# Kernel tuning notes

Hardware: AMD Instinct MI355X
Metric: run time of the kernel (lower is better)

## Reference

```python
import jax, jax.numpy as jnp
import numpy as np

N_NODES = 100000
N_EDGES = 1600000
IN_DIM = 128
HID = 64
N_CLASSES = 40
NEG_SLOPE = 0.2


def setup_inputs() -> dict:
    key = jax.random.key(0)
    ks = jax.random.split(key, 12)
    s_in = 1.0 / np.sqrt(IN_DIM)
    s_h = 1.0 / np.sqrt(HID)
    return {
        "x": jax.random.normal(ks[0], (N_NODES, IN_DIM), dtype=jnp.float32),
        "edge_index": jax.random.randint(ks[1], (2, N_EDGES), 0, N_NODES, dtype=jnp.int64),
        "W0": jax.random.normal(ks[2], (IN_DIM, HID), dtype=jnp.float32) * s_in,
        "a_s0": jax.random.normal(ks[3], (HID,), dtype=jnp.float32) * s_h,
        "a_d0": jax.random.normal(ks[4], (HID,), dtype=jnp.float32) * s_h,
        "b0": jnp.zeros((HID,), dtype=jnp.float32),
        "W1": jax.random.normal(ks[5], (HID, HID), dtype=jnp.float32) * s_h,
        "a_s1": jax.random.normal(ks[6], (HID,), dtype=jnp.float32) * s_h,
        "a_d1": jax.random.normal(ks[7], (HID,), dtype=jnp.float32) * s_h,
        "b1": jnp.zeros((HID,), dtype=jnp.float32),
        "Wl": jax.random.normal(ks[8], (HID, N_CLASSES), dtype=jnp.float32) * s_h,
        "bl": jnp.zeros((N_CLASSES,), dtype=jnp.float32),
    }


def gat_conv(x, src, dst, W, a_s, a_d, b, n_nodes):
    # single-head GATConv (PyG default heads=1), self-loops already in src/dst
    h = x @ W                                  # [N, d]
    e = jax.nn.leaky_relu((h @ a_s)[src] + (h @ a_d)[dst], NEG_SLOPE)  # [E]
    # segment softmax over incoming edges of each dst node
    m = jax.ops.segment_max(e, dst, num_segments=n_nodes)
    p = jnp.exp(e - m[dst])
    denom = jax.ops.segment_sum(p, dst, num_segments=n_nodes)
    alpha = p / (denom[dst] + 1e-16)           # [E]
    out = jax.ops.segment_sum(alpha[:, None] * h[src], dst, num_segments=n_nodes)
    return out + b


def reference(x, edge_index, W0, a_s0, a_d0, b0, W1, a_s1, a_d1, b1, Wl, bl):
    n = x.shape[0]
    loop = jnp.arange(n, dtype=edge_index.dtype)
    src = jnp.concatenate([edge_index[0], loop])
    dst = jnp.concatenate([edge_index[1], loop])
    h = gat_conv(x, src, dst, W0, a_s0, a_d0, b0, n)
    h = jax.nn.elu(h)
    h = gat_conv(h, src, dst, W1, a_s1, a_d1, b1, n)
    h = jax.nn.elu(h)
    return h @ Wl + bl
```

## Files before the change

kernel.cpp:

```cpp
#include <hip/hip_runtime.h>
#include <math.h>

#define NEG_SLOPE 0.2f
#define CAP 128
#define BSH 9
#define BSZ 512
#define CHUNK 4096
#define PADS 16
#define CAPQ 16384

typedef __attribute__((ext_vector_type(8))) short short8;
typedef __attribute__((ext_vector_type(4))) float f32x4;

__device__ __forceinline__ float hred_sum(float v) {
#pragma unroll
    for (int o = 16; o >= 1; o >>= 1) v += __shfl_xor(v, o, 64);
    return v;
}
__device__ __forceinline__ unsigned int f2bf(float f) {
    unsigned int u = __float_as_uint(f);
    return (u + 0x7fffu + ((u >> 16) & 1u)) >> 16;
}
__device__ __forceinline__ float bflo(unsigned int u) { return __uint_as_float(u << 16); }
__device__ __forceinline__ float bfhi(unsigned int u) { return __uint_as_float(u & 0xffff0000u); }


__global__ __launch_bounds__(256) void k_scatter(
        const int* __restrict__ src, const int* __restrict__ dst,
        int* __restrict__ bcursor, int* __restrict__ ebuf, int E) {
    __shared__ int lh[256], lb[256];
    const int tid = threadIdx.x;
    int base = blockIdx.x * CHUNK;
    int sv[16], dv[16];
    bool ok[16];
#pragma unroll
    for (int u = 0; u < 16; ++u) {
        int i = base + u * 256 + tid;
        ok[u] = i < E;
        int ii = ok[u] ? i : E - 1;
        dv[u] = dst[ii];
        sv[u] = src[ii];
    }
    lh[tid] = 0;
    __syncthreads();
#pragma unroll
    for (int u = 0; u < 16; ++u)
        if (ok[u]) atomicAdd(&lh[dv[u] >> BSH], 1);
    __syncthreads();
    int c = lh[tid];
    lb[tid] = c ? atomicAdd(&bcursor[tid * PADS], c) : 0;
    lh[tid] = 0;
    __syncthreads();
#pragma unroll
    for (int u = 0; u < 16; ++u) {
        if (ok[u]) {
            int d = dv[u], b = d >> BSH;
            int pp = atomicAdd(&lh[b], 1);
            int pos = lb[b] + pp;
            if (pos < CAPQ)
                ebuf[b * CAPQ + pos] = (sv[u] << BSH) | (d & (BSZ - 1));
        }
    }
}


__device__ __forceinline__ void gemm0_body(char* smem, int bid,
        const float* __restrict__ X, const float* __restrict__ W,
        const float* __restrict__ a_s, const float* __restrict__ a_d,
        unsigned int* __restrict__ hb, float* __restrict__ ss, float* __restrict__ sd, int N) {
    constexpr int K = 128, OUTW = 64, NKC = K / 32, NC = OUTW / 16;
    short* wfrag = (short*)smem;
    unsigned int* hs = (unsigned int*)(smem + 16384);

    const int tid  = threadIdx.x;
    const int lane = tid & 63;
    const int w    = tid >> 6;
    const int m    = lane & 15;
    const int q8   = lane >> 4;
    const int rowbase = bid * 128 + w * 16;

    for (int f = tid; f < NKC * NC * 64; f += 512) {
        int flane = f & 63;
        int fc    = (f >> 6) % NC;
        int fkc   = (f >> 6) / NC;
        int col   = fc * 16 + (flane & 15);
        int k0    = fkc * 32 + (flane >> 4) * 8;
        short8 b;
#pragma unroll
        for (int j = 0; j < 8; ++j) b[j] = (short)f2bf(W[(k0 + j) * OUTW + col]);
        *(short8*)&wfrag[f * 8] = b;
    }
    __syncthreads();

    int grow = rowbase + m; if (grow >= N) grow = N - 1;

    f32x4 acc[NC];
#pragma unroll
    for (int c = 0; c < NC; ++c) acc[c] = (f32x4)0.f;

    const float* xrow = X + (size_t)grow * K + q8 * 8;
#pragma unroll
    for (int kc = 0; kc < NKC; ++kc) {
        float4 v0 = *(const float4*)(xrow + kc * 32);
        float4 v1 = *(const float4*)(xrow + kc * 32 + 4);
        float vv[8] = {v0.x, v0.y, v0.z, v0.w, v1.x, v1.y, v1.z, v1.w};
        short8 ah, al;
#pragma unroll
        for (int j = 0; j < 8; ++j) {
            unsigned int hb16 = f2bf(vv[j]);
            ah[j] = (short)hb16;
            al[j] = (short)f2bf(vv[j] - __uint_as_float(hb16 << 16));
        }
#pragma unroll
        for (int c = 0; c < NC; ++c) {
            short8 b = *(short8*)&wfrag[((kc * NC + c) * 64 + lane) * 8];
            acc[c] = __builtin_amdgcn_mfma_f32_16x16x32_bf16(ah, b, acc[c], 0, 0, 0);
            acc[c] = __builtin_amdgcn_mfma_f32_16x16x32_bf16(al, b, acc[c], 0, 0, 0);
        }
    }

    float asv[NC], adv[NC];
#pragma unroll
    for (int c = 0; c < NC; ++c) { asv[c] = a_s[c * 16 + m]; adv[c] = a_d[c * 16 + m]; }
#pragma unroll
    for (int i = 0; i < 4; ++i) {
        float s = 0.f, d = 0.f;
#pragma unroll
        for (int c = 0; c < NC; ++c) {
            s = fmaf(acc[c][i], asv[c], s);
            d = fmaf(acc[c][i], adv[c], d);
        }
#pragma unroll
        for (int o = 1; o <= 8; o <<= 1) {
            s += __shfl_xor(s, o, 64);
            d += __shfl_xor(d, o, 64);
        }
        int r = rowbase + q8 * 4 + i;
        if (m == 0 && r < N) { ss[r] = s; sd[r] = d; }
    }

    unsigned short* hsw = (unsigned short*)&hs[w * 512];
#pragma unroll
    for (int c = 0; c < NC; ++c)
#pragma unroll
        for (int i = 0; i < 4; ++i)
            hsw[(q8 * 4 + i) * 64 + c * 16 + m] = (unsigned short)f2bf(acc[c][i]);
    unsigned int* hu = &hs[w * 512];
    int row = lane >> 2, u0 = (lane & 3) * 8;
    uint4 va = *(uint4*)&hu[row * 32 + u0];
    uint4 vb = *(uint4*)&hu[row * 32 + u0 + 4];
    int r = rowbase + row;
    if (r < N) {
        *(uint4*)&hb[(size_t)r * 32 + u0]     = va;
        *(uint4*)&hb[(size_t)r * 32 + u0 + 4] = vb;
    }
}

__device__ __forceinline__ void build_body(char* smem, int b,
        const int* __restrict__ bcursor, const int* __restrict__ ebuf,
        int* __restrict__ rowptr, int* __restrict__ csr,
        int N, int nbuck) {
    int* sdeg  = (int*)smem;
    int* sscan = sdeg + 512;
    int* shdr  = sscan + 512;
    const int t = threadIdx.x;

    int nlo = b << BSH;
    int cn = N - nlo; if (cn > BSZ) cn = BSZ;

    int bcv = 0, totv = 0;
    if (t < 256) {
        int cnb = 0;
        if (t < nbuck) {
            bcv = bcursor[t * PADS]; if (bcv > CAPQ) bcv = CAPQ;
            cnb = N - (t << BSH); if (cnb > BSZ) cnb = BSZ; if (cnb < 0) cnb = 0;
        }
        totv = bcv + cnb;
        sscan[t] = totv;
    }
    __syncthreads();
#pragma unroll
    for (int off = 1; off < 256; off <<= 1) {
        int u = 0;
        if (t < 256 && t >= off) u = sscan[t - off];
        __syncthreads();
        if (t < 256) sscan[t] += u;
        __syncthreads();
    }
    if (t == b) { shdr[0] = sscan[t] - totv; shdr[1] = bcv; }
    if (b == 0 && t == nbuck - 1) rowptr[N] = sscan[t];
    __syncthreads();
    int cb = shdr[0], ec = shdr[1];
    int e0 = b * CAPQ;

    sdeg[t] = (t < cn) ? 1 : 0;
    __syncthreads();
    {
        int i = t;
        for (; i + 1536 < ec; i += 2048) {
            int r0 = ebuf[e0 + i], r1 = ebuf[e0 + i + 512];
            int r2 = ebuf[e0 + i + 1024], r3 = ebuf[e0 + i + 1536];
            atomicAdd(&sdeg[r0 & (BSZ - 1)], 1);
            atomicAdd(&sdeg[r1 & (BSZ - 1)], 1);
            atomicAdd(&sdeg[r2 & (BSZ - 1)], 1);
            atomicAdd(&sdeg[r3 & (BSZ - 1)], 1);
        }
        for (; i < ec; i += 512)
            atomicAdd(&sdeg[ebuf[e0 + i] & (BSZ - 1)], 1);
    }
    __syncthreads();
    int v = sdeg[t];
    sscan[t] = v;
    __syncthreads();
#pragma unroll
    for (int off = 1; off < BSZ; off <<= 1) {
        int u = (t >= off) ? sscan[t - off] : 0;
        __syncthreads();
        sscan[t] += u;
        __syncthreads();
    }
    int excl = sscan[t] - v;
    if (t < cn) {
        rowptr[nlo + t] = cb + excl;
        csr[cb + excl] = nlo + t;
        sdeg[t] = excl + 1;
    }
    __syncthreads();
    {
        int i = t;
        for (; i + 1536 < ec; i += 2048) {
            int r0 = ebuf[e0 + i], r1 = ebuf[e0 + i + 512];
            int r2 = ebuf[e0 + i + 1024], r3 = ebuf[e0 + i + 1536];
            int p0 = atomicAdd(&sdeg[r0 & (BSZ - 1)], 1);
            int p1 = atomicAdd(&sdeg[r1 & (BSZ - 1)], 1);
            int p2 = atomicAdd(&sdeg[r2 & (BSZ - 1)], 1);
            int p3 = atomicAdd(&sdeg[r3 & (BSZ - 1)], 1);
            csr[cb + p0] = r0 >> BSH;
            csr[cb + p1] = r1 >> BSH;
            csr[cb + p2] = r2 >> BSH;
            csr[cb + p3] = r3 >> BSH;
        }
        for (; i < ec; i += 512) {
            int rec = ebuf[e0 + i];
            int p = atomicAdd(&sdeg[rec & (BSZ - 1)], 1);
            csr[cb + p] = rec >> BSH;
        }
    }
}

__global__ __launch_bounds__(512) void k_mid(
        int* __restrict__ bcursor, int* __restrict__ ebuf, int gbm, int nbuck,
        const float* __restrict__ X, const float* __restrict__ W,
        const float* __restrict__ a_s, const float* __restrict__ a_d,
        unsigned int* __restrict__ hb, float* __restrict__ ss, float* __restrict__ sd,
        int* __restrict__ rowptr, int* __restrict__ csr, int N) {
    __shared__ __align__(16) char smem[32768];
    int bid = blockIdx.x;
    if (bid < gbm)
        gemm0_body(smem, bid, X, W, a_s, a_d, hb, ss, sd, N);
    else
        build_body(smem, bid - gbm, bcursor, ebuf, rowptr, csr, N, nbuck);
}


template <int OUTW, bool LAST>
__global__ __launch_bounds__(512) void k_aggmm(
        const int* __restrict__ rowptr, const int* __restrict__ csr,
        const float* __restrict__ ss, const float* __restrict__ sd,
        const unsigned int* __restrict__ hb, const float* __restrict__ bias,
        const float* __restrict__ W, const float* __restrict__ a_s2,
        const float* __restrict__ a_d2,
        unsigned int* __restrict__ hbout, float* __restrict__ ssout,
        float* __restrict__ sdout,
        const float* __restrict__ bias2, float* __restrict__ fout, int N) {
    constexpr int NKC = 2;
    constexpr int NC  = (OUTW + 15) / 16;
    __shared__ __align__(16) short wfrag[NKC * NC * 64 * 8];
    __shared__ __align__(16) float sal[16][CAP];
    __shared__ __align__(16) int   sof[16][CAP];
    __shared__ __align__(16) short afrag[NKC][512];
    __shared__ __align__(16) unsigned short hsw[LAST ? 1 : 16][64];
    __shared__ float ssp[LAST ? 1 : NC][16], sdp[LAST ? 1 : NC][16];

    const int tid  = threadIdx.x;
    const int lane = tid & 63;
    const int w    = tid >> 6;
    const int m    = lane & 15;
    const int q8   = lane >> 4;

    for (int f = tid; f < NKC * NC * 64; f += 512) {
        int flane = f & 63;
        int fc    = (f >> 6) % NC;
        int fkc   = (f >> 6) / NC;
        int col   = fc * 16 + (flane & 15);
        int k0    = fkc * 32 + (flane >> 4) * 8;
        short8 b;
#pragma unroll
        for (int j = 0; j < 8; ++j) {
            float v = (col < OUTW) ? W[(k0 + j) * OUTW + col] : 0.f;
            b[j] = (short)f2bf(v);
        }
        *(short8*)&wfrag[f * 8] = b;
    }

    const int hw = tid >> 5;
    const int p  = tid & 31;
    const int nb = blockIdx.x * 16;
    const int n  = nb + hw;
    const bool valid = n < N;
    const char* hbb = (const char*)hb;
    const int p4 = p * 4;

    int ro = 0, deg = 0;
    float sdn = 0.f;
    if (valid) {
        ro  = rowptr[n];
        deg = rowptr[n + 1] - ro;
        sdn = sd[n];
    }

    float fxr, fyr, inv;
    if (deg <= CAP) {
        float sum = 0.f;
        for (int j = p; j < deg; j += 32) {
            int s = csr[ro + j];
            float e = ss[s] + sdn;
            e = fmaxf(e, NEG_SLOPE * e);
            float pe = __expf(e);
            sal[hw][j] = pe;
            sof[hw][j] = s << 7;
            sum += pe;
        }
        sum = hred_sum(sum);
        inv = 1.f / (sum + 1e-16f);

        float ax = 0.f, ay = 0.f, bx = 0.f, by = 0.f, cx = 0.f, cy = 0.f, dx = 0.f, dy = 0.f;
        int j = 0;
        for (; j + 7 < deg; j += 8) {
            float4 al0 = *(const float4*)&sal[hw][j];
            float4 al1 = *(const float4*)&sal[hw][j + 4];
            int4   of0 = *(const int4*)&sof[hw][j];
            int4   of1 = *(const int4*)&sof[hw][j + 4];
            unsigned int u0 = *(const unsigned int*)(hbb + (of0.x + p4));
            unsigned int u1 = *(const unsigned int*)(hbb + (of0.y + p4));
            unsigned int u2 = *(const unsigned int*)(hbb + (of0.z + p4));
            unsigned int u3 = *(const unsigned int*)(hbb + (of0.w + p4));
            unsigned int u4 = *(const unsigned int*)(hbb + (of1.x + p4));
            unsigned int u5 = *(const unsigned int*)(hbb + (of1.y + p4));
            unsigned int u6 = *(const unsigned int*)(hbb + (of1.z + p4));
            unsigned int u7 = *(const unsigned int*)(hbb + (of1.w + p4));
            ax = fmaf(bflo(u0), al0.x, ax); ay = fmaf(bfhi(u0), al0.x, ay);
            bx = fmaf(bflo(u1), al0.y, bx); by = fmaf(bfhi(u1), al0.y, by);
            cx = fmaf(bflo(u2), al0.z, cx); cy = fmaf(bfhi(u2), al0.z, cy);
            dx = fmaf(bflo(u3), al0.w, dx); dy = fmaf(bfhi(u3), al0.w, dy);
            ax = fmaf(bflo(u4), al1.x, ax); ay = fmaf(bfhi(u4), al1.x, ay);
            bx = fmaf(bflo(u5), al1.y, bx); by = fmaf(bfhi(u5), al1.y, by);
            cx = fmaf(bflo(u6), al1.z, cx); cy = fmaf(bfhi(u6), al1.z, cy);
            dx = fmaf(bflo(u7), al1.w, dx); dy = fmaf(bfhi(u7), al1.w, dy);
        }
        for (; j + 3 < deg; j += 4) {
            float4 al0 = *(const float4*)&sal[hw][j];
            int4   of0 = *(const int4*)&sof[hw][j];
            unsigned int u0 = *(const unsigned int*)(hbb + (of0.x + p4));
            unsigned int u1 = *(const unsigned int*)(hbb + (of0.y + p4));
            unsigned int u2 = *(const unsigned int*)(hbb + (of0.z + p4));
            unsigned int u3 = *(const unsigned int*)(hbb + (of0.w + p4));
            ax = fmaf(bflo(u0), al0.x, ax); ay = fmaf(bfhi(u0), al0.x, ay);
            bx = fmaf(bflo(u1), al0.y, bx); by = fmaf(bfhi(u1), al0.y, by);
            cx = fmaf(bflo(u2), al0.z, cx); cy = fmaf(bfhi(u2), al0.z, cy);
            dx = fmaf(bflo(u3), al0.w, dx); dy = fmaf(bfhi(u3), al0.w, dy);
        }
        for (; j < deg; ++j) {
            float a = sal[hw][j];
            unsigned int u0 = *(const unsigned int*)(hbb + (sof[hw][j] + p4));
            ax = fmaf(bflo(u0), a, ax); ay = fmaf(bfhi(u0), a, ay);
        }
        fxr = (ax + bx) + (cx + dx);
        fyr = (ay + by) + (cy + dy);
    } else {
        float sum = 0.f;
        for (int j = p; j < deg; j += 32) {
            int s = csr[ro + j];
            float e = ss[s] + sdn;
            e = fmaxf(e, NEG_SLOPE * e);
            sum += __expf(e);
        }
        sum = hred_sum(sum);
        inv = 1.f / (sum + 1e-16f);
        float fx = 0.f, fy = 0.f;
        for (int j = 0; j < deg; ++j) {
            int s = csr[ro + j];
            float e = ss[s] + sdn;
            e = fmaxf(e, NEG_SLOPE * e);
            float pe = __expf(e);
            unsigned int u = *(const unsigned int*)(hbb + ((s << 7) + p4));
            fx = fmaf(bflo(u), pe, fx); fy = fmaf(bfhi(u), pe, fy);
        }
        fxr = fx; fyr = fy;
    }
    {
        float2 ob = *(const float2*)&bias[p * 2];
        float ox = fmaf(fxr, inv, ob.x);
        float oy = fmaf(fyr, inv, ob.y);
        ox = (ox > 0.f) ? ox : __expf(ox) - 1.f;
        oy = (oy > 0.f) ? oy : __expf(oy) - 1.f;
        unsigned int zu = (f2bf(oy) << 16) | f2bf(ox);
        int k   = 2 * p;
        int kc  = k >> 5;
        int idx = ((((k & 31) >> 3) * 16 + hw) << 3) + (k & 7);
        *(unsigned int*)&afrag[kc][idx] = zu;
    }
    __syncthreads();

    if (w < NC) {
        f32x4 acc = (f32x4)0.f;
#pragma unroll
        for (int kc = 0; kc < NKC; ++kc) {
            short8 a = *(short8*)&afrag[kc][lane * 8];
            short8 b = *(short8*)&wfrag[((kc * NC + w) * 64 + lane) * 8];
            acc = __builtin_amdgcn_mfma_f32_16x16x32_bf16(a, b, acc, 0, 0, 0);
        }
        if constexpr (LAST) {
#pragma unroll
            for (int i = 0; i < 4; ++i) {
                int r = nb + q8 * 4 + i;
                int col = w * 16 + m;
                if (r < N && col < OUTW)
                    fout[(size_t)r * OUTW + col] = acc[i] + bias2[col];
            }
        } else {
            float asv = a_s2[w * 16 + m];
            float adv = a_d2[w * 16 + m];
#pragma unroll
            for (int i = 0; i < 4; ++i) {
                float s = acc[i] * asv, d = acc[i] * adv;
#pragma unroll
                for (int o = 1; o <= 8; o <<= 1) {
                    s += __shfl_xor(s, o, 64);
                    d += __shfl_xor(d, o, 64);
                }
                if (m == 0) { ssp[w][q8 * 4 + i] = s; sdp[w][q8 * 4 + i] = d; }
                hsw[q8 * 4 + i][w * 16 + m] = (unsigned short)f2bf(acc[i]);
            }
        }
    }
    if constexpr (!LAST) {
        __syncthreads();
        if (tid < 16) {
            int r = nb + tid;
            if (r < N) {
                float s = 0.f, d = 0.f;
#pragma unroll
                for (int c = 0; c < NC; ++c) { s += ssp[c][tid]; d += sdp[c][tid]; }
                ssout[r] = s; sdout[r] = d;
            }
        }
        if (tid < 128) {
            int row = tid >> 3, seg = tid & 7;
            int r = nb + row;
            if (r < N) {
                uint4 v = *(uint4*)&((unsigned int*)hsw)[row * 32 + seg * 4];
                *(uint4*)&hbout[(size_t)r * 32 + seg * 4] = v;
            }
        }
    }
}


extern "C" void kernel_launch(void* const* d_in, const int* in_sizes, int n_in,
                              void* d_out, int out_size, void* d_ws, size_t ws_size,
                              hipStream_t stream) {
    const float* x   = (const float*)d_in[0];
    const int*   ei  = (const int*)d_in[1];
    const float* W0  = (const float*)d_in[2];
    const float* as0 = (const float*)d_in[3];
    const float* ad0 = (const float*)d_in[4];
    const float* b0  = (const float*)d_in[5];
    const float* W1  = (const float*)d_in[6];
    const float* as1 = (const float*)d_in[7];
    const float* ad1 = (const float*)d_in[8];
    const float* b1  = (const float*)d_in[9];
    const float* Wl  = (const float*)d_in[10];
    const float* bl  = (const float*)d_in[11];
    float* out = (float*)d_out;

    int N = in_sizes[0] / 128;
    int E = in_sizes[1] / 2;
    const int* srcp = ei;
    const int* dstp = ei + E;
    int nbuck = (N + BSZ - 1) >> BSH;

    char* wp = (char*)d_ws;
    auto alloc = [&](size_t bytes) { void* p = (void*)wp; wp += (bytes + 255) & ~(size_t)255; return p; };
    unsigned int* hb0 = (unsigned int*)alloc((size_t)N * 32 * 4);
    unsigned int* hb1 = (unsigned int*)alloc((size_t)N * 32 * 4);
    float* ss0     = (float*)alloc((size_t)N * 4);
    float* sd0     = (float*)alloc((size_t)N * 4);
    float* ss1     = (float*)alloc((size_t)N * 4);
    float* sd1     = (float*)alloc((size_t)N * 4);
    int*   rowptr  = (int*)alloc((size_t)(N + 1) * 4);
    int*   csr     = (int*)alloc((size_t)(E + N) * 4);
    int*   ebuf    = (int*)alloc((size_t)nbuck * CAPQ * 4);
    int*   bcursor = (int*)alloc(256 * PADS * 4);

    int nscat = (E + CHUNK - 1) / CHUNK;
    int gbm = (N + 127) / 128;
    int gagg = (N + 15) / 16;

    hipMemsetAsync(bcursor, 0, 256 * PADS * 4, stream);
    k_scatter<<<nscat, 256, 0, stream>>>(srcp, dstp, bcursor, ebuf, E);
    k_mid<<<gbm + nbuck, 512, 0, stream>>>(bcursor, ebuf, gbm, nbuck,
                                           x, W0, as0, ad0, hb0, ss0, sd0,
                                           rowptr, csr, N);

    k_aggmm<64, false><<<gagg, 512, 0, stream>>>(rowptr, csr, ss0, sd0, hb0, b0,
                                                 W1, as1, ad1,
                                                 hb1, ss1, sd1, nullptr, nullptr, N);
    k_aggmm<40, true><<<gagg, 512, 0, stream>>>(rowptr, csr, ss1, sd1, hb1, b1,
                                                Wl, nullptr, nullptr,
                                                nullptr, nullptr, nullptr, bl, out, N);
}
```

Baseline: 240.4 us.

## Fuse all GAT stages into one persistent cooperative kernel with grid syncs

Replaces the memset plus four separate kernel launches with a single cooperative persistent kernel that runs scatter, GEMM0/CSR build, and both aggregate-matmul layers in grid-stride loops, separated by grid.sync(). The aim is to remove launch overhead and the inter-kernel gaps. In exchange, occupancy is capped at a grid of at most 1024 blocks, which can reduce latency hiding on the gather-heavy aggregation phases. Grid-wide barriers also have their own cost. The old multi-kernel path is kept as a fallback if the cooperative launch fails.

```diff
diff --git a/kernel.cpp b/kernel.cpp
--- a/kernel.cpp
+++ b/kernel.cpp
@@ -1,5 +1,8 @@
 #include <hip/hip_runtime.h>
+#include <hip/hip_cooperative_groups.h>
 #include <math.h>
+
+namespace cg = cooperative_groups;
 
 #define NEG_SLOPE 0.2f
 #define CAP 128
@@ -24,6 +27,48 @@
 __device__ __forceinline__ float bflo(unsigned int u) { return __uint_as_float(u << 16); }
 __device__ __forceinline__ float bfhi(unsigned int u) { return __uint_as_float(u & 0xffff0000u); }
 
+
+__device__ __forceinline__ void scatter512_body(char* smemraw, int bid,
+        const int* __restrict__ src, const int* __restrict__ dst,
+        int* __restrict__ bcursor, int* __restrict__ ebuf, int E) {
+    int* lh = (int*)smemraw;
+    int* lb = lh + 256;
+    const int tid = threadIdx.x;
+    int base = bid * CHUNK;
+    int sv[8], dv[8];
+    bool ok[8];
+#pragma unroll
+    for (int u = 0; u < 8; ++u) {
+        int i = base + u * 512 + tid;
+        ok[u] = i < E;
+        int ii = ok[u] ? i : E - 1;
+        dv[u] = dst[ii];
+        sv[u] = src[ii];
+    }
+    if (tid < 256) lh[tid] = 0;
+    __syncthreads();
+#pragma unroll
+    for (int u = 0; u < 8; ++u)
+        if (ok[u]) atomicAdd(&lh[dv[u] >> BSH], 1);
+    __syncthreads();
+    if (tid < 256) {
+        int c = lh[tid];
+        lb[tid] = c ? atomicAdd(&bcursor[tid * PADS], c) : 0;
+        lh[tid] = 0;
+    }
+    __syncthreads();
+#pragma unroll
+    for (int u = 0; u < 8; ++u) {
+        if (ok[u]) {
+            int d = dv[u], b = d >> BSH;
+            int pp = atomicAdd(&lh[b], 1);
+            int pos = lb[b] + pp;
+            if (pos < CAPQ)
+                ebuf[b * CAPQ + pos] = (sv[u] << BSH) | (d & (BSZ - 1));
+        }
+    }
+    __syncthreads();
+}
 
 __global__ __launch_bounds__(256) void k_scatter(
         const int* __restrict__ src, const int* __restrict__ dst,
@@ -62,7 +107,6 @@
         }
     }
 }
-
 
 __device__ __forceinline__ void gemm0_body(char* smem, int bid,
         const float* __restrict__ X, const float* __restrict__ W,
@@ -248,6 +292,258 @@
     }
 }
 
+
+template <int OUTW, bool LAST>
+__device__ __forceinline__ void aggmm_phase(char* smemraw, int bid, int nblk, int gagg,
+        const int* __restrict__ rowptr, const int* __restrict__ csr,
+        const float* __restrict__ ss, const float* __restrict__ sd,
+        const unsigned int* __restrict__ hb, const float* __restrict__ bias,
+        const float* __restrict__ W, const float* __restrict__ a_s2,
+        const float* __restrict__ a_d2,
+        unsigned int* __restrict__ hbout, float* __restrict__ ssout,
+        float* __restrict__ sdout,
+        const float* __restrict__ bias2, float* __restrict__ fout, int N) {
+    constexpr int NKC = 2;
+    constexpr int NC  = (OUTW + 15) / 16;
+    constexpr int WB  = NKC * NC * 64 * 8 * 2;
+    short* wfrag = (short*)smemraw;
+    float (*sal)[CAP]   = (float(*)[CAP])(smemraw + WB);
+    int   (*sof)[CAP]   = (int(*)[CAP])(smemraw + WB + 16 * CAP * 4);
+    short (*afrag)[512] = (short(*)[512])(smemraw + WB + 2 * 16 * CAP * 4);
+    unsigned short* hsw = (unsigned short*)(smemraw + WB + 2 * 16 * CAP * 4 + NKC * 512 * 2);
+    float (*ssp)[16] = (float(*)[16])(smemraw + WB + 2 * 16 * CAP * 4 + NKC * 512 * 2 + 16 * 64 * 2);
+    float (*sdp)[16] = (float(*)[16])((char*)ssp + NC * 16 * 4);
+
+    const int tid  = threadIdx.x;
+    const int lane = tid & 63;
+    const int w    = tid >> 6;
+    const int m    = lane & 15;
+    const int q8   = lane >> 4;
+    const int hw   = tid >> 5;
+    const int p    = tid & 31;
+    const int p4   = p * 4;
+    const char* hbb = (const char*)hb;
+
+    for (int f = tid; f < NKC * NC * 64; f += 512) {
+        int flane = f & 63;
+        int fc    = (f >> 6) % NC;
+        int fkc   = (f >> 6) / NC;
+        int col   = fc * 16 + (flane & 15);
+        int k0    = fkc * 32 + (flane >> 4) * 8;
+        short8 b;
+#pragma unroll
+        for (int j = 0; j < 8; ++j) {
+            float v = (col < OUTW) ? W[(k0 + j) * OUTW + col] : 0.f;
+            b[j] = (short)f2bf(v);
+        }
+        *(short8*)&wfrag[f * 8] = b;
+    }
+    __syncthreads();
+
+    for (int tile = bid; tile < gagg; tile += nblk) {
+        const int nb = tile * 16;
+        const int n  = nb + hw;
+        const bool valid = n < N;
+
+        int ro = 0, deg = 0;
+        float sdn = 0.f;
+        if (valid) {
+            ro  = rowptr[n];
+            deg = rowptr[n + 1] - ro;
+            sdn = sd[n];
+        }
+
+        float fxr, fyr, inv;
+        if (deg <= CAP) {
+            float sum = 0.f;
+            for (int j = p; j < deg; j += 32) {
+                int s = csr[ro + j];
+                float e = ss[s] + sdn;
+                e = fmaxf(e, NEG_SLOPE * e);
+                float pe = __expf(e);
+                sal[hw][j] = pe;
+                sof[hw][j] = s << 7;
+                sum += pe;
+            }
+            sum = hred_sum(sum);
+            inv = 1.f / (sum + 1e-16f);
+
+            float ax = 0.f, ay = 0.f, bx = 0.f, by = 0.f, cx = 0.f, cy = 0.f, dx = 0.f, dy = 0.f;
+            int j = 0;
+            for (; j + 7 < deg; j += 8) {
+                float4 al0 = *(const float4*)&sal[hw][j];
+                float4 al1 = *(const float4*)&sal[hw][j + 4];
+                int4   of0 = *(const int4*)&sof[hw][j];
+                int4   of1 = *(const int4*)&sof[hw][j + 4];
+                unsigned int u0 = *(const unsigned int*)(hbb + (of0.x + p4));
+                unsigned int u1 = *(const unsigned int*)(hbb + (of0.y + p4));
+                unsigned int u2 = *(const unsigned int*)(hbb + (of0.z + p4));
+                unsigned int u3 = *(const unsigned int*)(hbb + (of0.w + p4));
+                unsigned int u4 = *(const unsigned int*)(hbb + (of1.x + p4));
+                unsigned int u5 = *(const unsigned int*)(hbb + (of1.y + p4));
+                unsigned int u6 = *(const unsigned int*)(hbb + (of1.z + p4));
+                unsigned int u7 = *(const unsigned int*)(hbb + (of1.w + p4));
+                ax = fmaf(bflo(u0), al0.x, ax); ay = fmaf(bfhi(u0), al0.x, ay);
+                bx = fmaf(bflo(u1), al0.y, bx); by = fmaf(bfhi(u1), al0.y, by);
+                cx = fmaf(bflo(u2), al0.z, cx); cy = fmaf(bfhi(u2), al0.z, cy);
+                dx = fmaf(bflo(u3), al0.w, dx); dy = fmaf(bfhi(u3), al0.w, dy);
+                ax = fmaf(bflo(u4), al1.x, ax); ay = fmaf(bfhi(u4), al1.x, ay);
+                bx = fmaf(bflo(u5), al1.y, bx); by = fmaf(bfhi(u5), al1.y, by);
+                cx = fmaf(bflo(u6), al1.z, cx); cy = fmaf(bfhi(u6), al1.z, cy);
+                dx = fmaf(bflo(u7), al1.w, dx); dy = fmaf(bfhi(u7), al1.w, dy);
+            }
+            for (; j + 3 < deg; j += 4) {
+                float4 al0 = *(const float4*)&sal[hw][j];
+                int4   of0 = *(const int4*)&sof[hw][j];
+                unsigned int u0 = *(const unsigned int*)(hbb + (of0.x + p4));
+                unsigned int u1 = *(const unsigned int*)(hbb + (of0.y + p4));
+                unsigned int u2 = *(const unsigned int*)(hbb + (of0.z + p4));
+                unsigned int u3 = *(const unsigned int*)(hbb + (of0.w + p4));
+                ax = fmaf(bflo(u0), al0.x, ax); ay = fmaf(bfhi(u0), al0.x, ay);
+                bx = fmaf(bflo(u1), al0.y, bx); by = fmaf(bfhi(u1), al0.y, by);
+                cx = fmaf(bflo(u2), al0.z, cx); cy = fmaf(bfhi(u2), al0.z, cy);
+                dx = fmaf(bflo(u3), al0.w, dx); dy = fmaf(bfhi(u3), al0.w, dy);
+            }
+            for (; j < deg; ++j) {
+                float a = sal[hw][j];
+                unsigned int u0 = *(const unsigned int*)(hbb + (sof[hw][j] + p4));
+                ax = fmaf(bflo(u0), a, ax); ay = fmaf(bfhi(u0), a, ay);
+            }
+            fxr = (ax + bx) + (cx + dx);
+            fyr = (ay + by) + (cy + dy);
+        } else {
+            float sum = 0.f;
+            for (int j = p; j < deg; j += 32) {
+                int s = csr[ro + j];
+                float e = ss[s] + sdn;
+                e = fmaxf(e, NEG_SLOPE * e);
+                sum += __expf(e);
+            }
+            sum = hred_sum(sum);
+            inv = 1.f / (sum + 1e-16f);
+            float fx = 0.f, fy = 0.f;
+            for (int j = 0; j < deg; ++j) {
+                int s = csr[ro + j];
+                float e = ss[s] + sdn;
+                e = fmaxf(e, NEG_SLOPE * e);
+                float pe = __expf(e);
+                unsigned int u = *(const unsigned int*)(hbb + ((s << 7) + p4));
+                fx = fmaf(bflo(u), pe, fx); fy = fmaf(bfhi(u), pe, fy);
+            }
+            fxr = fx; fyr = fy;
+        }
+        {
+            float2 ob = *(const float2*)&bias[p * 2];
+            float ox = fmaf(fxr, inv, ob.x);
+            float oy = fmaf(fyr, inv, ob.y);
+            ox = (ox > 0.f) ? ox : __expf(ox) - 1.f;
+            oy = (oy > 0.f) ? oy : __expf(oy) - 1.f;
+            unsigned int zu = (f2bf(oy) << 16) | f2bf(ox);
+            int k   = 2 * p;
+            int kc  = k >> 5;
+            int idx = ((((k & 31) >> 3) * 16 + hw) << 3) + (k & 7);
+            *(unsigned int*)&afrag[kc][idx] = zu;
+        }
+        __syncthreads();
+
+        if (w < NC) {
+            f32x4 acc = (f32x4)0.f;
+#pragma unroll
+            for (int kc = 0; kc < NKC; ++kc) {
+                short8 a = *(short8*)&afrag[kc][lane * 8];
+                short8 b = *(short8*)&wfrag[((kc * NC + w) * 64 + lane) * 8];
+                acc = __builtin_amdgcn_mfma_f32_16x16x32_bf16(a, b, acc, 0, 0, 0);
+            }
+            if constexpr (LAST) {
+#pragma unroll
+                for (int i = 0; i < 4; ++i) {
+                    int r = nb + q8 * 4 + i;
+                    int col = w * 16 + m;
+                    if (r < N && col < OUTW)
+                        fout[(size_t)r * OUTW + col] = acc[i] + bias2[col];
+                }
+            } else {
+                float asv = a_s2[w * 16 + m];
+                float adv = a_d2[w * 16 + m];
+#pragma unroll
+                for (int i = 0; i < 4; ++i) {
+                    float s = acc[i] * asv, d = acc[i] * adv;
+#pragma unroll
+                    for (int o = 1; o <= 8; o <<= 1) {
+                        s += __shfl_xor(s, o, 64);
+                        d += __shfl_xor(d, o, 64);
+                    }
+                    if (m == 0) { ssp[w][q8 * 4 + i] = s; sdp[w][q8 * 4 + i] = d; }
+                    hsw[(q8 * 4 + i) * 64 + w * 16 + m] = (unsigned short)f2bf(acc[i]);
+                }
+            }
+        }
+        if constexpr (!LAST) {
+            __syncthreads();
+            if (tid < 16) {
+                int r = nb + tid;
+                if (r < N) {
+                    float s = 0.f, d = 0.f;
+#pragma unroll
+                    for (int c = 0; c < NC; ++c) { s += ssp[c][tid]; d += sdp[c][tid]; }
+                    ssout[r] = s; sdout[r] = d;
+                }
+            }
+            if (tid < 128) {
+                int row = tid >> 3, seg = tid & 7;
+                int r = nb + row;
+                if (r < N) {
+                    uint4 v = *(uint4*)&((unsigned int*)hsw)[row * 32 + seg * 4];
+                    *(uint4*)&hbout[(size_t)r * 32 + seg * 4] = v;
+                }
+            }
+        }
+        __syncthreads();
+    }
+}
+
+
+__global__ __launch_bounds__(512) void k_all(
+        const int* __restrict__ src, const int* __restrict__ dst,
+        int* __restrict__ bcursor, int* __restrict__ ebuf,
+        int E, int nscat, int gbm, int nbuck,
+        const float* __restrict__ x, const float* __restrict__ W0,
+        const float* __restrict__ as0, const float* __restrict__ ad0,
+        unsigned int* __restrict__ hb0, float* __restrict__ ss0, float* __restrict__ sd0,
+        int* __restrict__ rowptr, int* __restrict__ csr,
+        const float* __restrict__ b0, const float* __restrict__ W1,
+        const float* __restrict__ as1, const float* __restrict__ ad1,
+        unsigned int* __restrict__ hb1, float* __restrict__ ss1, float* __restrict__ sd1,
+        const float* __restrict__ b1, const float* __restrict__ Wl,
+        const float* __restrict__ bl, float* __restrict__ out, int gagg, int N) {
+    __shared__ __align__(16) char smem[32768];
+    cg::grid_group grid = cg::this_grid();
+    const int bid = blockIdx.x, nblk = gridDim.x, tid = threadIdx.x;
+
+    if (bid == 0)
+        for (int i = tid; i < 256 * PADS; i += 512) bcursor[i] = 0;
+    grid.sync();
+
+    for (int c = bid; c < nscat; c += nblk)
+        scatter512_body(smem, c, src, dst, bcursor, ebuf, E);
+    grid.sync();
+
+    for (int r = bid; r < gbm + nbuck; r += nblk) {
+        if (r < gbm) gemm0_body(smem, r, x, W0, as0, ad0, hb0, ss0, sd0, N);
+        else         build_body(smem, r - gbm, bcursor, ebuf, rowptr, csr, N, nbuck);
+        __syncthreads();
+    }
+    grid.sync();
+
+    aggmm_phase<64, false>(smem, bid, nblk, gagg, rowptr, csr, ss0, sd0, hb0, b0,
+                           W1, as1, ad1, hb1, ss1, sd1, nullptr, nullptr, N);
+    grid.sync();
+
+    aggmm_phase<40, true>(smem, bid, nblk, gagg, rowptr, csr, ss1, sd1, hb1, b1,
+                          Wl, nullptr, nullptr, nullptr, nullptr, nullptr, bl, out, N);
+}
+
+
 __global__ __launch_bounds__(512) void k_mid(
         int* __restrict__ bcursor, int* __restrict__ ebuf, int gbm, int nbuck,
         const float* __restrict__ X, const float* __restrict__ W,
@@ -262,7 +558,6 @@
         build_body(smem, bid - gbm, bcursor, ebuf, rowptr, csr, N, nbuck);
 }
 
-
 template <int OUTW, bool LAST>
 __global__ __launch_bounds__(512) void k_aggmm(
         const int* __restrict__ rowptr, const int* __restrict__ csr,
@@ -273,197 +568,10 @@
         unsigned int* __restrict__ hbout, float* __restrict__ ssout,
         float* __restrict__ sdout,
         const float* __restrict__ bias2, float* __restrict__ fout, int N) {
-    constexpr int NKC = 2;
-    constexpr int NC  = (OUTW + 15) / 16;
-    __shared__ __align__(16) short wfrag[NKC * NC * 64 * 8];
-    __shared__ __align__(16) float sal[16][CAP];
-    __shared__ __align__(16) int   sof[16][CAP];
-    __shared__ __align__(16) short afrag[NKC][512];
-    __shared__ __align__(16) unsigned short hsw[LAST ? 1 : 16][64];
-    __shared__ float ssp[LAST ? 1 : NC][16], sdp[LAST ? 1 : NC][16];
-
-    const int tid  = threadIdx.x;
-    const int lane = tid & 63;
-    const int w    = tid >> 6;
-    const int m    = lane & 15;
-    const int q8   = lane >> 4;
-
-    for (int f = tid; f < NKC * NC * 64; f += 512) {
-        int flane = f & 63;
-        int fc    = (f >> 6) % NC;
-        int fkc   = (f >> 6) / NC;
-        int col   = fc * 16 + (flane & 15);
-        int k0    = fkc * 32 + (flane >> 4) * 8;
-        short8 b;
-#pragma unroll
-        for (int j = 0; j < 8; ++j) {
-            float v = (col < OUTW) ? W[(k0 + j) * OUTW + col] : 0.f;
-            b[j] = (short)f2bf(v);
-        }
-        *(short8*)&wfrag[f * 8] = b;
-    }
-
-    const int hw = tid >> 5;
-    const int p  = tid & 31;
-    const int nb = blockIdx.x * 16;
-    const int n  = nb + hw;
-    const bool valid = n < N;
-    const char* hbb = (const char*)hb;
-    const int p4 = p * 4;
-
-    int ro = 0, deg = 0;
-    float sdn = 0.f;
-    if (valid) {
-        ro  = rowptr[n];
-        deg = rowptr[n + 1] - ro;
-        sdn = sd[n];
-    }
-
-    float fxr, fyr, inv;
-    if (deg <= CAP) {
-        float sum = 0.f;
-        for (int j = p; j < deg; j += 32) {
-            int s = csr[ro + j];
-            float e = ss[s] + sdn;
-            e = fmaxf(e, NEG_SLOPE * e);
-            float pe = __expf(e);
-            sal[hw][j] = pe;
-            sof[hw][j] = s << 7;
-            sum += pe;
-        }
-        sum = hred_sum(sum);
-        inv = 1.f / (sum + 1e-16f);
-
-        float ax = 0.f, ay = 0.f, bx = 0.f, by = 0.f, cx = 0.f, cy = 0.f, dx = 0.f, dy = 0.f;
-        int j = 0;
-        for (; j + 7 < deg; j += 8) {
-            float4 al0 = *(const float4*)&sal[hw][j];
-            float4 al1 = *(const float4*)&sal[hw][j + 4];
-            int4   of0 = *(const int4*)&sof[hw][j];
-            int4   of1 = *(const int4*)&sof[hw][j + 4];
-            unsigned int u0 = *(const unsigned int*)(hbb + (of0.x + p4));
-            unsigned int u1 = *(const unsigned int*)(hbb + (of0.y + p4));
-            unsigned int u2 = *(const unsigned int*)(hbb + (of0.z + p4));
-            unsigned int u3 = *(const unsigned int*)(hbb + (of0.w + p4));
-            unsigned int u4 = *(const unsigned int*)(hbb + (of1.x + p4));
-            unsigned int u5 = *(const unsigned int*)(hbb + (of1.y + p4));
-            unsigned int u6 = *(const unsigned int*)(hbb + (of1.z + p4));
-            unsigned int u7 = *(const unsigned int*)(hbb + (of1.w + p4));
-            ax = fmaf(bflo(u0), al0.x, ax); ay = fmaf(bfhi(u0), al0.x, ay);
-            bx = fmaf(bflo(u1), al0.y, bx); by = fmaf(bfhi(u1), al0.y, by);
-            cx = fmaf(bflo(u2), al0.z, cx); cy = fmaf(bfhi(u2), al0.z, cy);
-            dx = fmaf(bflo(u3), al0.w, dx); dy = fmaf(bfhi(u3), al0.w, dy);
-            ax = fmaf(bflo(u4), al1.x, ax); ay = fmaf(bfhi(u4), al1.x, ay);
-            bx = fmaf(bflo(u5), al1.y, bx); by = fmaf(bfhi(u5), al1.y, by);
-            cx = fmaf(bflo(u6), al1.z, cx); cy = fmaf(bfhi(u6), al1.z, cy);
-            dx = fmaf(bflo(u7), al1.w, dx); dy = fmaf(bfhi(u7), al1.w, dy);
-        }
-        for (; j + 3 < deg; j += 4) {
-            float4 al0 = *(const float4*)&sal[hw][j];
-            int4   of0 = *(const int4*)&sof[hw][j];
-            unsigned int u0 = *(const unsigned int*)(hbb + (of0.x + p4));
-            unsigned int u1 = *(const unsigned int*)(hbb + (of0.y + p4));
-            unsigned int u2 = *(const unsigned int*)(hbb + (of0.z + p4));
-            unsigned int u3 = *(const unsigned int*)(hbb + (of0.w + p4));
-            ax = fmaf(bflo(u0), al0.x, ax); ay = fmaf(bfhi(u0), al0.x, ay);
-            bx = fmaf(bflo(u1), al0.y, bx); by = fmaf(bfhi(u1), al0.y, by);
-            cx = fmaf(bflo(u2), al0.z, cx); cy = fmaf(bfhi(u2), al0.z, cy);
-            dx = fmaf(bflo(u3), al0.w, dx); dy = fmaf(bfhi(u3), al0.w, dy);
-        }
-        for (; j < deg; ++j) {
-            float a = sal[hw][j];
-            unsigned int u0 = *(const unsigned int*)(hbb + (sof[hw][j] + p4));
-            ax = fmaf(bflo(u0), a, ax); ay = fmaf(bfhi(u0), a, ay);
-        }
-        fxr = (ax + bx) + (cx + dx);
-        fyr = (ay + by) + (cy + dy);
-    } else {
-        float sum = 0.f;
-        for (int j = p; j < deg; j += 32) {
-            int s = csr[ro + j];
-            float e = ss[s] + sdn;
-            e = fmaxf(e, NEG_SLOPE * e);
-            sum += __expf(e);
-        }
-        sum = hred_sum(sum);
-        inv = 1.f / (sum + 1e-16f);
-        float fx = 0.f, fy = 0.f;
-        for (int j = 0; j < deg; ++j) {
-            int s = csr[ro + j];
-            float e = ss[s] + sdn;
-            e = fmaxf(e, NEG_SLOPE * e);
-            float pe = __expf(e);
-            unsigned int u = *(const unsigned int*)(hbb + ((s << 7) + p4));
-            fx = fmaf(bflo(u), pe, fx); fy = fmaf(bfhi(u), pe, fy);
-        }
-        fxr = fx; fyr = fy;
-    }
-    {
-        float2 ob = *(const float2*)&bias[p * 2];
-        float ox = fmaf(fxr, inv, ob.x);
-        float oy = fmaf(fyr, inv, ob.y);
-        ox = (ox > 0.f) ? ox : __expf(ox) - 1.f;
-        oy = (oy > 0.f) ? oy : __expf(oy) - 1.f;
-        unsigned int zu = (f2bf(oy) << 16) | f2bf(ox);
-        int k   = 2 * p;
-        int kc  = k >> 5;
-        int idx = ((((k & 31) >> 3) * 16 + hw) << 3) + (k & 7);
-        *(unsigned int*)&afrag[kc][idx] = zu;
-    }
-    __syncthreads();
-
-    if (w < NC) {
-        f32x4 acc = (f32x4)0.f;
-#pragma unroll
-        for (int kc = 0; kc < NKC; ++kc) {
-            short8 a = *(short8*)&afrag[kc][lane * 8];
-            short8 b = *(short8*)&wfrag[((kc * NC + w) * 64 + lane) * 8];
-            acc = __builtin_amdgcn_mfma_f32_16x16x32_bf16(a, b, acc, 0, 0, 0);
-        }
-        if constexpr (LAST) {
-#pragma unroll
-            for (int i = 0; i < 4; ++i) {
-                int r = nb + q8 * 4 + i;
-                int col = w * 16 + m;
-                if (r < N && col < OUTW)
-                    fout[(size_t)r * OUTW + col] = acc[i] + bias2[col];
-            }
-        } else {
-            float asv = a_s2[w * 16 + m];
-            float adv = a_d2[w * 16 + m];
-#pragma unroll
-            for (int i = 0; i < 4; ++i) {
-                float s = acc[i] * asv, d = acc[i] * adv;
-#pragma unroll
-                for (int o = 1; o <= 8; o <<= 1) {
-                    s += __shfl_xor(s, o, 64);
-                    d += __shfl_xor(d, o, 64);
-                }
-                if (m == 0) { ssp[w][q8 * 4 + i] = s; sdp[w][q8 * 4 + i] = d; }
-                hsw[q8 * 4 + i][w * 16 + m] = (unsigned short)f2bf(acc[i]);
-            }
-        }
-    }
-    if constexpr (!LAST) {
-        __syncthreads();
-        if (tid < 16) {
-            int r = nb + tid;
-            if (r < N) {
-                float s = 0.f, d = 0.f;
-#pragma unroll
-                for (int c = 0; c < NC; ++c) { s += ssp[c][tid]; d += sdp[c][tid]; }
-                ssout[r] = s; sdout[r] = d;
-            }
-        }
-        if (tid < 128) {
-            int row = tid >> 3, seg = tid & 7;
-            int r = nb + row;
-            if (r < N) {
-                uint4 v = *(uint4*)&((unsigned int*)hsw)[row * 32 + seg * 4];
-                *(uint4*)&hbout[(size_t)r * 32 + seg * 4] = v;
-            }
-        }
-    }
+    __shared__ __align__(16) char smem[32768];
+    aggmm_phase<OUTW, LAST>(smem, blockIdx.x, gridDim.x, blockIdx.x + 1,
+                            rowptr, csr, ss, sd, hb, bias, W, a_s2, a_d2,
+                            hbout, ssout, sdout, bias2, fout, N);
 }
 
 
@@ -504,15 +612,35 @@
     int*   bcursor = (int*)alloc(256 * PADS * 4);
 
     int nscat = (E + CHUNK - 1) / CHUNK;
-    int gbm = (N + 127) / 128;
-    int gagg = (N + 15) / 16;
+    int gbm   = (N + 127) / 128;
+    int gagg  = (N + 15) / 16;
+
+    int occ = 0;
+    hipError_t qerr = hipOccupancyMaxActiveBlocksPerMultiprocessor(
+        &occ, reinterpret_cast<const void*>(k_all), 512, 0);
+    if (qerr == hipSuccess && occ > 0) {
+        int grid = occ * 256;
+        if (grid > 1024) grid = 1024;
+        void* kargs[] = { (void*)&srcp, (void*)&dstp, (void*)&bcursor, (void*)&ebuf,
+                          (void*)&E, (void*)&nscat, (void*)&gbm, (void*)&nbuck,
+                          (void*)&x, (void*)&W0, (void*)&as0, (void*)&ad0,
+                          (void*)&hb0, (void*)&ss0, (void*)&sd0,
+                          (void*)&rowptr, (void*)&csr,
+                          (void*)&b0, (void*)&W1, (void*)&as1, (void*)&ad1,
+                          (void*)&hb1, (void*)&ss1, (void*)&sd1,
+                          (void*)&b1, (void*)&Wl, (void*)&bl,
+                          (void*)&out, (void*)&gagg, (void*)&N };
+        hipError_t ce = hipLaunchCooperativeKernel(
+            reinterpret_cast<const void*>(k_all), dim3(grid), dim3(512), kargs, 0, stream);
+        if (ce == hipSuccess) return;
+        (void)hipGetLastError();
+    }
 
     hipMemsetAsync(bcursor, 0, 256 * PADS * 4, stream);
     k_scatter<<<nscat, 256, 0, stream>>>(srcp, dstp, bcursor, ebuf, E);
     k_mid<<<gbm + nbuck, 512, 0, stream>>>(bcursor, ebuf, gbm, nbuck,
                                            x, W0, as0, ad0, hb0, ss0, sd0,
                                            rowptr, csr, N);
-
     k_aggmm<64, false><<<gagg, 512, 0, stream>>>(rowptr, csr, ss0, sd0, hb0, b0,
                                                  W1, as1, ad1,
                                                  hb1, ss1, sd1, nullptr, nullptr, N);
```

Result: slower. 502.5 us (+109.0%).
